# Optimization experiments

Measured on AMD Instinct MI355X. Metric: run time of the kernel, lower is better.

Reference implementation:

```python
import jax, jax.numpy as jnp
import numpy as np

B, N, D_IN, D_OUT, NUM_RING = 32, 8192, 64, 128, 4
BN_EPS = 1e-5


def setup_inputs() -> dict:
    key = jax.random.key(0)
    ks = jax.random.split(key, 8)
    return {
        "x": jax.random.normal(ks[0], (B, D_IN, N), dtype=jnp.float32),
        "ring": jax.random.randint(ks[1], (B, N), 0, NUM_RING, dtype=jnp.int64),
        "W": jax.random.normal(ks[2], (NUM_RING, D_OUT, D_IN), dtype=jnp.float32) * 0.1,
        "b": jax.random.normal(ks[3], (NUM_RING, D_OUT), dtype=jnp.float32) * 0.1,
        "gamma": jax.random.uniform(ks[4], (NUM_RING, D_OUT), dtype=jnp.float32) + 0.5,
        "beta": jax.random.normal(ks[5], (NUM_RING, D_OUT), dtype=jnp.float32) * 0.1,
        "mean": jax.random.normal(ks[6], (NUM_RING, D_OUT), dtype=jnp.float32) * 0.1,
        "var": jax.random.uniform(ks[7], (NUM_RING, D_OUT), dtype=jnp.float32) + 0.5,
    }


def reference(x, ring, W, b, gamma, beta, mean, var):
    # x: [B, 64, N]; ring: [B, N] int labels in [0, num_ring)
    xt = jnp.transpose(x, (0, 2, 1))  # [B, N, 64]
    Bv, Nv, _ = xt.shape
    num_ring = W.shape[0]
    out = jnp.zeros((Bv, Nv, W.shape[1]), dtype=x.dtype)
    neg = jnp.finfo(x.dtype).min
    for i in range(num_ring):  # small fixed loop over rings
        # 1x1 conv == per-point linear, then BatchNorm (inference-mode affine)
        y = jnp.einsum("bnd,od->bno", xt, W[i]) + b[i]  # [B, N, 128]
        scale = gamma[i] * jax.lax.rsqrt(var[i] + BN_EPS)
        y = (y - mean[i]) * scale + beta[i]
        m = (ring == i)[..., None]  # [B, N, 1]
        # per-(batch, ring) segment max over points, broadcast back to members
        ymax = jnp.max(jnp.where(m, y, neg), axis=1, keepdims=True)  # [B, 1, 128]
        out = jnp.where(m, ymax, out)
    return jnp.transpose(out, (0, 2, 1))  # [B, 128, N]
```

## Files before the change

kernel.cpp:

```cpp
#include <hip/hip_runtime.h>
#include <hip/hip_bf16.h>
#include <cstdint>
#include <cstddef>

#define BB 32
#define NN 8192
#define DIN 64
#define DOUT 128
#define NR 4
#define BN_EPS 1e-5f
#define CHUNKS 32

typedef float nfloat4 __attribute__((ext_vector_type(4)));
typedef float floatx4 __attribute__((ext_vector_type(4)));
typedef short short8 __attribute__((ext_vector_type(8)));


__device__ inline void pack2(float a, float b, short8& dst, int idx) {
  __hip_bfloat162 h = __float22bfloat162_rn(make_float2(a, b));
  const unsigned int bits = *(unsigned int*)&h;
  dst[idx] = (short)(bits & 0xffffu);
  dst[idx + 1] = (short)(bits >> 16);
}

__device__ inline int swz(int n) { return (n ^ (n >> 2) ^ (n >> 5)) & 7; }

__global__ void __launch_bounds__(256) k_compute(
    const float* __restrict__ x, const float* __restrict__ W,
    const int* __restrict__ ring, float* __restrict__ part) {
  const int b = blockIdx.y;
  const int cx = blockIdx.x;
  const int n0 = cx * 256;
  const int wave = (int)threadIdx.x >> 6;
  const int lane = (int)threadIdx.x & 63;
  const int quad = lane >> 4;
  const int l16 = lane & 15;
  const float* xb = x + (size_t)b * DIN * NN;
  const int* rgb = ring + (size_t)b * NN;

  __shared__ short8 lx[256 * 8];

  {
    const float* xr = xb + (size_t)(wave * 16) * NN + n0 + 4 * lane;
#pragma unroll
    for (int grp = 0; grp < 2; ++grp) {
      nfloat4 L[8];
#pragma unroll
      for (int j = 0; j < 8; ++j)
        L[j] = *(const nfloat4*)&xr[(size_t)(grp * 8 + j) * NN];
#pragma unroll
      for (int i = 0; i < 4; ++i) {
        short8 v;
        pack2(L[0][i], L[1][i], v, 0);
        pack2(L[2][i], L[3][i], v, 2);
        pack2(L[4][i], L[5][i], v, 4);
        pack2(L[6][i], L[7][i], v, 6);
        const int ni = 4 * lane + i;
        lx[ni * 8 + ((wave * 2 + grp) ^ swz(ni))] = v;
      }
    }
  }

  short8 afr[NR][2][2];
#pragma unroll
  for (int r = 0; r < NR; ++r) {
#pragma unroll
    for (int tt = 0; tt < 2; ++tt) {
      const int chan = (wave + 4 * tt) * 16 + l16;
      const float* wr = W + ((size_t)r * DOUT + chan) * DIN + quad * 8;
#pragma unroll
      for (int ks = 0; ks < 2; ++ks) {
        const float4 w0 = *(const float4*)&wr[ks * 32];
        const float4 w1 = *(const float4*)&wr[ks * 32 + 4];
        short8 a;
        pack2(w0.x, w0.y, a, 0);
        pack2(w0.z, w0.w, a, 2);
        pack2(w1.x, w1.y, a, 4);
        pack2(w1.z, w1.w, a, 6);
        afr[r][tt][ks] = a;
      }
    }
  }

  floatx4 rmax[2][NR];
#pragma unroll
  for (int tt = 0; tt < 2; ++tt)
#pragma unroll
    for (int r = 0; r < NR; ++r)
      rmax[tt][r] = {-INFINITY, -INFINITY, -INFINITY, -INFINITY};

  __syncthreads();

#pragma unroll 4
  for (int T = 0; T < 16; ++T) {
    const int n = T * 16 + l16;
    const short8 b0 = lx[n * 8 + (quad ^ swz(n))];
    const short8 b1 = lx[n * 8 + ((4 + quad) ^ swz(n))];
    const int rr = rgb[n0 + n];
#pragma unroll
    for (int r = 0; r < NR; ++r) {
      floatx4 acc0 = {0.f, 0.f, 0.f, 0.f};
      floatx4 acc1 = {0.f, 0.f, 0.f, 0.f};
      acc0 = __builtin_amdgcn_mfma_f32_16x16x32_bf16(afr[r][0][0], b0, acc0, 0, 0, 0);
      acc0 = __builtin_amdgcn_mfma_f32_16x16x32_bf16(afr[r][0][1], b1, acc0, 0, 0, 0);
      acc1 = __builtin_amdgcn_mfma_f32_16x16x32_bf16(afr[r][1][0], b0, acc1, 0, 0, 0);
      acc1 = __builtin_amdgcn_mfma_f32_16x16x32_bf16(afr[r][1][1], b1, acc1, 0, 0, 0);
      if (rr == r) {
#pragma unroll
        for (int p = 0; p < 4; ++p) {
          rmax[0][r][p] = fmaxf(rmax[0][r][p], acc0[p]);
          rmax[1][r][p] = fmaxf(rmax[1][r][p], acc1[p]);
        }
      }
    }
  }

  float* slot = part + (size_t)(b * CHUNKS + cx) * NR * DOUT;
#pragma unroll
  for (int tt = 0; tt < 2; ++tt) {
#pragma unroll
    for (int r = 0; r < NR; ++r) {
#pragma unroll
      for (int p = 0; p < 4; ++p) {
        float v = rmax[tt][r][p];
        v = fmaxf(v, __shfl_xor(v, 1, 64));
        v = fmaxf(v, __shfl_xor(v, 2, 64));
        v = fmaxf(v, __shfl_xor(v, 4, 64));
        v = fmaxf(v, __shfl_xor(v, 8, 64));
        if (l16 == 0) {
          const int chan = (wave + 4 * tt) * 16 + quad * 4 + p;
          slot[r * DOUT + chan] = v;
        }
      }
    }
  }
}

__global__ void __launch_bounds__(256) k_out(
    const float* __restrict__ bias, const float* __restrict__ gamma,
    const float* __restrict__ beta, const float* __restrict__ mean,
    const float* __restrict__ var, const int* __restrict__ ring,
    const float* __restrict__ part, float* __restrict__ out) {
  const int b = blockIdx.z;
  const int og = blockIdx.y;
  const int n0 = blockIdx.x * 1024;
  const int t = (int)threadIdx.x;

  __shared__ float lut[32 * NR * 32];
  {
    const int oo = t >> 3;
    const int r = (t >> 1) & 3;
    const int c0 = (t & 1) * 16;
    const int o = og * 32 + oo;
    const float* ps = part + (size_t)b * CHUNKS * NR * DOUT + r * DOUT + o;
    float raw = -INFINITY;
#pragma unroll
    for (int c = 0; c < CHUNKS; ++c)
      raw = fmaxf(raw, ps[(size_t)c * NR * DOUT]);
    const int tt = r * DOUT + o;
    const float sc = gamma[tt] * rsqrtf(var[tt] + BN_EPS);
    const float val = (raw + bias[tt] - mean[tt]) * sc + beta[tt];
    nfloat4 v4 = {val, val, val, val};
    float* dst = &lut[(oo * NR + r) * 32 + c0];
#pragma unroll
    for (int k = 0; k < 4; ++k) *(nfloat4*)&dst[k * 4] = v4;
  }
  __syncthreads();

  const int n = n0 + t * 4;
  const int4 rg = *(const int4*)&ring[(size_t)b * NN + n];
  const int l31 = t & 31;
  const float* p0 = &lut[rg.x * 32 + l31];
  const float* p1 = &lut[rg.y * 32 + l31];
  const float* p2 = &lut[rg.z * 32 + l31];
  const float* p3 = &lut[rg.w * 32 + l31];
  float* orow = out + ((size_t)b * DOUT + og * 32) * NN + n;

#pragma unroll 8
  for (int oo = 0; oo < 32; ++oo) {
    nfloat4 v;
    v.x = p0[oo * 128];
    v.y = p1[oo * 128];
    v.z = p2[oo * 128];
    v.w = p3[oo * 128];
    *(nfloat4*)(orow + (size_t)oo * NN) = v;
  }
}

extern "C" void kernel_launch(void* const* d_in, const int* in_sizes, int n_in,
                              void* d_out, int out_size, void* d_ws, size_t ws_size,
                              hipStream_t stream) {
  const float* x = (const float*)d_in[0];
  const int* ring = (const int*)d_in[1];
  const float* W = (const float*)d_in[2];
  const float* bias = (const float*)d_in[3];
  const float* gamma = (const float*)d_in[4];
  const float* beta = (const float*)d_in[5];
  const float* mean = (const float*)d_in[6];
  const float* var = (const float*)d_in[7];
  float* out = (float*)d_out;

  float* part = (float*)d_ws;

  k_compute<<<dim3(CHUNKS, BB), 256, 0, stream>>>(x, W, ring, part);
  k_out<<<dim3(NN / 1024, DOUT / 32, BB), 256, 0, stream>>>(bias, gamma, beta, mean,
                                                            var, ring, part, out);
}
```

Baseline: 233.5 us.

## Double-buffer x tiles in larger compute blocks with fewer partial chunks

The compute kernel now runs 512-thread blocks that each cover 1024 points in four 256-point sub-chunks. The next chunk of x is loaded into registers while MFMAs run on the current chunk in a double-buffered LDS tile. Each wave now owns a single 16-channel output tile and packs 8 input rows. This cuts the partial-max slots per batch from 32 to 8, so the output kernel has less reduction work. The trade-off is a grid of only 256 blocks, which lowers occupancy and parallelism in exchange for load/compute overlap and less reloading of W per block.

```diff
diff --git a/kernel.cpp b/kernel.cpp
--- a/kernel.cpp
+++ b/kernel.cpp
@@ -9,7 +9,7 @@
 #define DOUT 128
 #define NR 4
 #define BN_EPS 1e-5f
-#define CHUNKS 32
+#define CHUNKS 8
 
 typedef float nfloat4 __attribute__((ext_vector_type(4)));
 typedef float floatx4 __attribute__((ext_vector_type(4)));
@@ -25,112 +25,114 @@
 
 __device__ inline int swz(int n) { return (n ^ (n >> 2) ^ (n >> 5)) & 7; }
 
-__global__ void __launch_bounds__(256) k_compute(
+__global__ void __launch_bounds__(512) k_compute(
     const float* __restrict__ x, const float* __restrict__ W,
     const int* __restrict__ ring, float* __restrict__ part) {
   const int b = blockIdx.y;
-  const int cx = blockIdx.x;
-  const int n0 = cx * 256;
-  const int wave = (int)threadIdx.x >> 6;
-  const int lane = (int)threadIdx.x & 63;
+  const int big = blockIdx.x;
+  const int n0 = big * 1024;
+  const int tid = (int)threadIdx.x;
+  const int wave = tid >> 6;
+  const int lane = tid & 63;
   const int quad = lane >> 4;
   const int l16 = lane & 15;
   const float* xb = x + (size_t)b * DIN * NN;
-  const int* rgb = ring + (size_t)b * NN;
-
-  __shared__ short8 lx[256 * 8];
-
-  {
-    const float* xr = xb + (size_t)(wave * 16) * NN + n0 + 4 * lane;
-#pragma unroll
-    for (int grp = 0; grp < 2; ++grp) {
-      nfloat4 L[8];
-#pragma unroll
-      for (int j = 0; j < 8; ++j)
-        L[j] = *(const nfloat4*)&xr[(size_t)(grp * 8 + j) * NN];
-#pragma unroll
-      for (int i = 0; i < 4; ++i) {
-        short8 v;
-        pack2(L[0][i], L[1][i], v, 0);
-        pack2(L[2][i], L[3][i], v, 2);
-        pack2(L[4][i], L[5][i], v, 4);
-        pack2(L[6][i], L[7][i], v, 6);
-        const int ni = 4 * lane + i;
-        lx[ni * 8 + ((wave * 2 + grp) ^ swz(ni))] = v;
-      }
-    }
-  }
-
-  short8 afr[NR][2][2];
+  const int* rgb = ring + (size_t)b * NN + n0;
+
+  __shared__ short8 lx[2][256 * 8];
+
+  short8 afr[NR][2];
 #pragma unroll
   for (int r = 0; r < NR; ++r) {
-#pragma unroll
-    for (int tt = 0; tt < 2; ++tt) {
-      const int chan = (wave + 4 * tt) * 16 + l16;
-      const float* wr = W + ((size_t)r * DOUT + chan) * DIN + quad * 8;
-#pragma unroll
-      for (int ks = 0; ks < 2; ++ks) {
-        const float4 w0 = *(const float4*)&wr[ks * 32];
-        const float4 w1 = *(const float4*)&wr[ks * 32 + 4];
-        short8 a;
-        pack2(w0.x, w0.y, a, 0);
-        pack2(w0.z, w0.w, a, 2);
-        pack2(w1.x, w1.y, a, 4);
-        pack2(w1.z, w1.w, a, 6);
-        afr[r][tt][ks] = a;
-      }
-    }
-  }
-
-  floatx4 rmax[2][NR];
-#pragma unroll
-  for (int tt = 0; tt < 2; ++tt)
-#pragma unroll
-    for (int r = 0; r < NR; ++r)
-      rmax[tt][r] = {-INFINITY, -INFINITY, -INFINITY, -INFINITY};
-
-  __syncthreads();
-
+    const int chan = wave * 16 + l16;
+    const float* wr = W + ((size_t)r * DOUT + chan) * DIN + quad * 8;
+#pragma unroll
+    for (int ks = 0; ks < 2; ++ks) {
+      const float4 w0 = *(const float4*)&wr[ks * 32];
+      const float4 w1 = *(const float4*)&wr[ks * 32 + 4];
+      short8 a;
+      pack2(w0.x, w0.y, a, 0);
+      pack2(w0.z, w0.w, a, 2);
+      pack2(w1.x, w1.y, a, 4);
+      pack2(w1.z, w1.w, a, 6);
+      afr[r][ks] = a;
+    }
+  }
+
+  floatx4 rmax[NR];
+#pragma unroll
+  for (int r = 0; r < NR; ++r)
+    rmax[r] = {-INFINITY, -INFINITY, -INFINITY, -INFINITY};
+
+  auto LOADL = [&](nfloat4 (&L)[8], int c) {
+    const float* base = xb + (size_t)(wave * 8) * NN + n0 + c * 256 + 4 * lane;
+#pragma unroll
+    for (int j = 0; j < 8; ++j)
+      L[j] = *(const nfloat4*)&base[(size_t)j * NN];
+  };
+  auto PACKW = [&](int buf, const nfloat4 (&L)[8]) {
+#pragma unroll
+    for (int i = 0; i < 4; ++i) {
+      short8 v;
+      pack2(L[0][i], L[1][i], v, 0);
+      pack2(L[2][i], L[3][i], v, 2);
+      pack2(L[4][i], L[5][i], v, 4);
+      pack2(L[6][i], L[7][i], v, 6);
+      const int ni = 4 * lane + i;
+      lx[buf][ni * 8 + (wave ^ swz(ni))] = v;
+    }
+  };
+  auto TLOOP = [&](int buf, int c) {
 #pragma unroll 4
-  for (int T = 0; T < 16; ++T) {
-    const int n = T * 16 + l16;
-    const short8 b0 = lx[n * 8 + (quad ^ swz(n))];
-    const short8 b1 = lx[n * 8 + ((4 + quad) ^ swz(n))];
-    const int rr = rgb[n0 + n];
-#pragma unroll
-    for (int r = 0; r < NR; ++r) {
-      floatx4 acc0 = {0.f, 0.f, 0.f, 0.f};
-      floatx4 acc1 = {0.f, 0.f, 0.f, 0.f};
-      acc0 = __builtin_amdgcn_mfma_f32_16x16x32_bf16(afr[r][0][0], b0, acc0, 0, 0, 0);
-      acc0 = __builtin_amdgcn_mfma_f32_16x16x32_bf16(afr[r][0][1], b1, acc0, 0, 0, 0);
-      acc1 = __builtin_amdgcn_mfma_f32_16x16x32_bf16(afr[r][1][0], b0, acc1, 0, 0, 0);
-      acc1 = __builtin_amdgcn_mfma_f32_16x16x32_bf16(afr[r][1][1], b1, acc1, 0, 0, 0);
-      if (rr == r) {
-#pragma unroll
-        for (int p = 0; p < 4; ++p) {
-          rmax[0][r][p] = fmaxf(rmax[0][r][p], acc0[p]);
-          rmax[1][r][p] = fmaxf(rmax[1][r][p], acc1[p]);
+    for (int T = 0; T < 16; ++T) {
+      const int n = T * 16 + l16;
+      const short8 b0 = lx[buf][n * 8 + (quad ^ swz(n))];
+      const short8 b1 = lx[buf][n * 8 + ((4 + quad) ^ swz(n))];
+      const int rr = rgb[c * 256 + n];
+#pragma unroll
+      for (int r = 0; r < NR; ++r) {
+        floatx4 acc = {0.f, 0.f, 0.f, 0.f};
+        acc = __builtin_amdgcn_mfma_f32_16x16x32_bf16(afr[r][0], b0, acc, 0, 0, 0);
+        acc = __builtin_amdgcn_mfma_f32_16x16x32_bf16(afr[r][1], b1, acc, 0, 0, 0);
+        if (rr == r) {
+#pragma unroll
+          for (int p = 0; p < 4; ++p) rmax[r][p] = fmaxf(rmax[r][p], acc[p]);
         }
       }
     }
-  }
-
-  float* slot = part + (size_t)(b * CHUNKS + cx) * NR * DOUT;
-#pragma unroll
-  for (int tt = 0; tt < 2; ++tt) {
-#pragma unroll
-    for (int r = 0; r < NR; ++r) {
-#pragma unroll
-      for (int p = 0; p < 4; ++p) {
-        float v = rmax[tt][r][p];
-        v = fmaxf(v, __shfl_xor(v, 1, 64));
-        v = fmaxf(v, __shfl_xor(v, 2, 64));
-        v = fmaxf(v, __shfl_xor(v, 4, 64));
-        v = fmaxf(v, __shfl_xor(v, 8, 64));
-        if (l16 == 0) {
-          const int chan = (wave + 4 * tt) * 16 + quad * 4 + p;
-          slot[r * DOUT + chan] = v;
-        }
+  };
+
+  nfloat4 LA[8], LB[8];
+  LOADL(LA, 0);
+  PACKW(0, LA);
+  LOADL(LB, 1);
+  __syncthreads();
+  TLOOP(0, 0);
+  PACKW(1, LB);
+  LOADL(LA, 2);
+  __syncthreads();
+  TLOOP(1, 1);
+  PACKW(0, LA);
+  LOADL(LB, 3);
+  __syncthreads();
+  TLOOP(0, 2);
+  PACKW(1, LB);
+  __syncthreads();
+  TLOOP(1, 3);
+
+  float* slot = part + (size_t)(b * CHUNKS + big) * NR * DOUT;
+#pragma unroll
+  for (int r = 0; r < NR; ++r) {
+#pragma unroll
+    for (int p = 0; p < 4; ++p) {
+      float v = rmax[r][p];
+      v = fmaxf(v, __shfl_xor(v, 1, 64));
+      v = fmaxf(v, __shfl_xor(v, 2, 64));
+      v = fmaxf(v, __shfl_xor(v, 4, 64));
+      v = fmaxf(v, __shfl_xor(v, 8, 64));
+      if (l16 == 0) {
+        const int chan = wave * 16 + quad * 4 + p;
+        slot[r * DOUT + chan] = v;
       }
     }
   }
@@ -202,7 +204,7 @@
 
   float* part = (float*)d_ws;
 
-  k_compute<<<dim3(CHUNKS, BB), 256, 0, stream>>>(x, W, ring, part);
+  k_compute<<<dim3(NN / 1024, BB), 512, 0, stream>>>(x, W, ring, part);
   k_out<<<dim3(NN / 1024, DOUT / 32, BB), 256, 0, stream>>>(bias, gamma, beta, mean,
                                                             var, ring, part, out);
 }
```

Result: faster. 225.9 us (-3.3%).
